# Performance work log

Hardware: AMD Instinct MI355X
Metric: run time of the kernel (lower is better)

Reference implementation:

```python
import jax, jax.numpy as jnp
import numpy as np

DIM = 256
HEADS = 8
WS = 16      # window size
WN = 16      # num windows (img 64x64)
KS = 3
B = 16
IMG = 64


def setup_inputs() -> dict:
    key = jax.random.key(0)
    ks = jax.random.split(key, 12)
    d = DIM
    hid = d // 16  # SE hidden (d >= 64)
    inp = {
        "x": jax.random.normal(ks[0], (B, d, IMG, IMG), dtype=jnp.float32),
        "conv_w": jax.random.normal(ks[1], (WN, d, d, KS, KS), dtype=jnp.float32) * 0.02,
        "wqkv": jax.random.normal(ks[2], (d, 3 * d), dtype=jnp.float32) * 0.02,
        "bqkv": jax.random.normal(ks[3], (3 * d,), dtype=jnp.float32) * 0.02,
        "wout": jax.random.normal(ks[4], (d, d), dtype=jnp.float32) * 0.02,
        "bout": jax.random.normal(ks[5], (d,), dtype=jnp.float32) * 0.02,
        "se_w1": jax.random.normal(ks[6], (WN, hid, d), dtype=jnp.float32) * 0.05,
        "se_b1": jax.random.normal(ks[7], (WN, hid), dtype=jnp.float32) * 0.02,
        "se_w2": jax.random.normal(ks[8], (WN, d, hid), dtype=jnp.float32) * 0.05,
        "se_b2": jax.random.normal(ks[9], (WN, d), dtype=jnp.float32) * 0.02,
        "ln_g": jnp.ones((d,), dtype=jnp.float32),
        "ln_b": jnp.zeros((d,), dtype=jnp.float32),
    }
    return inp


def reference(x, conv_w, wqkv, bqkv, wout, bout, se_w1, se_b1, se_w2, se_b2, ln_g, ln_b):
    Bn, C, H, W = x.shape
    hd = C // HEADS
    scale = hd ** (-0.5)

    # window partition: (WN, B, C, WS, WS), windows in (h_idx, w_idx) row-major order
    xw = x.reshape(Bn, C, H // WS, WS, W // WS, WS).transpose(2, 4, 0, 1, 3, 5)
    xw = xw.reshape(WN, Bn, C, WS, WS)

    # kernel tokens: per-layer weight.view(B, C, -1).permute(0,2,1), cat on axis 1
    last = C * KS * KS // Bn
    kt = conv_w.reshape(WN, Bn, C, last).transpose(1, 0, 3, 2).reshape(Bn, WN * last, C)

    # self-attention over kernel tokens (batch axis becomes dim C after reshape)
    qkv = kt @ wqkv + bqkv                                    # (B, WN*last, 3C)
    qkv = qkv.reshape(C, WN * KS * KS, 3, HEADS, hd).transpose(2, 0, 3, 1, 4)
    q, k, v = qkv[0] * scale, qkv[1], qkv[2]                  # (C, H, T, hd), T = WN*KS*KS
    attn = jax.nn.softmax(jnp.einsum('dhqe,dhke->dhqk', q, k), axis=-1)
    o = jnp.einsum('dhqk,dhke->dhqe', attn, v)
    o = o.transpose(0, 2, 1, 3).reshape(C, WN * KS * KS, C)
    o = o @ wout + bout
    kern = o.reshape(C, WN, KS, KS, C).transpose(1, 0, 4, 2, 3)  # (WN, Cout, Cin, KS, KS)

    # SE gating per window: kernels[i] treated as (batch=C, channels=C, KS, KS)
    pooled = kern.mean(axis=(3, 4))                            # (WN, C, C)
    h = jax.nn.relu(jnp.einsum('wbc,whc->wbh', pooled, se_w1) + se_b1[:, None, :])
    s = jax.nn.sigmoid(jnp.einsum('wbh,wch->wbc', h, se_w2) + se_b2[:, None, :])
    kern = kern * s[:, :, :, None, None]

    # per-window conv as a single grouped conv (groups = WN)
    xg = xw.transpose(1, 0, 2, 3, 4).reshape(Bn, WN * C, WS, WS)
    wg = kern.reshape(WN * C, C, KS, KS)
    yg = jax.lax.conv_general_dilated(xg, wg, (1, 1), ((1, 1), (1, 1)),
                                      feature_group_count=WN)
    yw = yg.reshape(Bn, WN, C, WS, WS).transpose(1, 0, 2, 3, 4)  # (WN, B, C, WS, WS)

    # window reverse
    y = yw.reshape(H // WS, W // WS, Bn, C, WS, WS).transpose(2, 3, 0, 4, 1, 5)
    y = y.reshape(Bn, C, H, W)

    # channel layernorm (eps=1e-5) + residual
    yn = y.transpose(0, 2, 3, 1)
    mu = yn.mean(-1, keepdims=True)
    var = ((yn - mu) ** 2).mean(-1, keepdims=True)
    yn = (yn - mu) / jnp.sqrt(var + 1e-5) * ln_g + ln_b
    return x + yn.transpose(0, 3, 1, 2)
```

## Files before the change

### kernel.cpp

```cpp
#include <hip/hip_runtime.h>

typedef __bf16 bf16;
typedef __bf16 bf16x8 __attribute__((ext_vector_type(8)));
typedef _Float16 f16;
typedef _Float16 f16x8 __attribute__((ext_vector_type(8)));
typedef float f32x4 __attribute__((ext_vector_type(4)));

#define SCALE_Q 0.17677669529663687f
#define KSCALE 64.0f
#define KSCALE_INV 0.015625f

__global__ __launch_bounds__(256) void k_prep_w(const float* __restrict__ wqkv,
                                                const float* __restrict__ wout,
                                                bf16* __restrict__ wqkv_t,
                                                f16* __restrict__ wout_h,
                                                f16* __restrict__ wout_l) {
    int n = blockIdx.x, k = threadIdx.x;
    if (n < 768) {
        wqkv_t[n * 256 + k] = (bf16)wqkv[k * 768 + n];
    } else {
        float f = wout[k * 256 + (n - 768)] * KSCALE;
        f16 hi = (f16)f;
        wout_h[(n - 768) * 256 + k] = hi;
        wout_l[(n - 768) * 256 + k] = (f16)(f - (float)hi);
    }
}

__global__ __launch_bounds__(256) void k_build_kt(const float* __restrict__ conv_w,
                                                  bf16* __restrict__ kt) {
    __shared__ float lds[2304];
    int w = blockIdx.x >> 8, co = blockIdx.x & 255;
    const float* src = conv_w + (size_t)(w * 256 + co) * 2304;
    for (int i = threadIdx.x; i < 2304; i += 256) lds[i] = src[i];
    __syncthreads();
    int b = co >> 4, c0 = (co & 15) << 4;
    size_t rbase = (size_t)(b * 16 + w) * 144;
    for (int i = threadIdx.x; i < 2304; i += 256) {
        int t = i >> 4, m = i & 15;
        kt[(rbase + t) * 256 + c0 + m] = (bf16)lds[m * 144 + t];
    }
}

typedef const __attribute__((address_space(1))) unsigned int* gas_t;
typedef __attribute__((address_space(3))) unsigned int* las_t;

__device__ __forceinline__ void async_copy16(const void* g, void* l) {
    __builtin_amdgcn_global_load_lds((gas_t)g, (las_t)l, 16, 0, 0);
}

__device__ __forceinline__ void mfma_tile_bf16(const bf16* As, const bf16* Bs,
                                               f32x4 acc[4][4]) {
    int lane = threadIdx.x & 63;
    int wave = threadIdx.x >> 6;
    int wm = (wave >> 1) * 64, wn = (wave & 1) * 64;
    int lrow = lane & 15, quad = lane >> 4;
    bf16x8 af[4], bfr[4];
#pragma unroll
    for (int i = 0; i < 4; i++) {
        int r = wm + i * 16 + lrow;
        af[i] = *(const bf16x8*)(As + r * 32 + ((quad ^ ((r >> 1) & 3)) << 3));
        int n = wn + i * 16 + lrow;
        bfr[i] = *(const bf16x8*)(Bs + n * 32 + ((quad ^ ((n >> 1) & 3)) << 3));
    }
#pragma unroll
    for (int i = 0; i < 4; i++)
#pragma unroll
        for (int j = 0; j < 4; j++)
            acc[i][j] = __builtin_amdgcn_mfma_f32_16x16x32_bf16(af[i], bfr[j], acc[i][j], 0, 0, 0);
}

__device__ __forceinline__ void mfma_tile_f16_dual(const f16* As, const f16* Bhs,
                                                   const f16* Bls, f32x4 acc[4][4]) {
    int lane = threadIdx.x & 63;
    int wave = threadIdx.x >> 6;
    int wm = (wave >> 1) * 64, wn = (wave & 1) * 64;
    int lrow = lane & 15, quad = lane >> 4;
    f16x8 af[4], bh[4], bl[4];
#pragma unroll
    for (int i = 0; i < 4; i++) {
        int r = wm + i * 16 + lrow;
        af[i] = *(const f16x8*)(As + r * 32 + ((quad ^ ((r >> 1) & 3)) << 3));
        int n = wn + i * 16 + lrow;
        bh[i] = *(const f16x8*)(Bhs + n * 32 + ((quad ^ ((n >> 1) & 3)) << 3));
        bl[i] = *(const f16x8*)(Bls + n * 32 + ((quad ^ ((n >> 1) & 3)) << 3));
    }
#pragma unroll
    for (int i = 0; i < 4; i++)
#pragma unroll
        for (int j = 0; j < 4; j++) {
            acc[i][j] = __builtin_amdgcn_mfma_f32_16x16x32_f16(af[i], bh[j], acc[i][j], 0, 0, 0);
            acc[i][j] = __builtin_amdgcn_mfma_f32_16x16x32_f16(af[i], bl[j], acc[i][j], 0, 0, 0);
        }
}

__device__ __forceinline__ void mfma_tile_f16_dual8(const f16* As, const f16* Bhs,
                                                    const f16* Bls, f32x4 acc[8][4]) {
    int lane = threadIdx.x & 63;
    int wave = threadIdx.x >> 6;
    int wm = (wave >> 1) * 128, wn = (wave & 1) * 64;
    int lrow = lane & 15, quad = lane >> 4;
    f16x8 af[8], bh[4], bl[4];
#pragma unroll
    for (int i = 0; i < 8; i++) {
        int r = wm + i * 16 + lrow;
        af[i] = *(const f16x8*)(As + r * 32 + ((quad ^ ((r >> 1) & 3)) << 3));
    }
#pragma unroll
    for (int j = 0; j < 4; j++) {
        int n = wn + j * 16 + lrow;
        bh[j] = *(const f16x8*)(Bhs + n * 32 + ((quad ^ ((n >> 1) & 3)) << 3));
        bl[j] = *(const f16x8*)(Bls + n * 32 + ((quad ^ ((n >> 1) & 3)) << 3));
    }
#pragma unroll
    for (int i = 0; i < 8; i++)
#pragma unroll
        for (int j = 0; j < 4; j++) {
            acc[i][j] = __builtin_amdgcn_mfma_f32_16x16x32_f16(af[i], bh[j], acc[i][j], 0, 0, 0);
            acc[i][j] = __builtin_amdgcn_mfma_f32_16x16x32_f16(af[i], bl[j], acc[i][j], 0, 0, 0);
        }
}

__global__ __launch_bounds__(256) void k_gemm_qkv(const bf16* __restrict__ A,
                                                  const bf16* __restrict__ Bt,
                                                  const float* __restrict__ bias,
                                                  bf16* __restrict__ outb,
                                                  int N, int K) {
    __shared__ __align__(16) bf16 As[2][128 * 32];
    __shared__ __align__(16) bf16 Bs[2][128 * 32];
    int m0 = blockIdx.y * 128, n0 = blockIdx.x * 128;
    int t = threadIdx.x, wave = t >> 6, lane = t & 63;
    int chunk0 = wave * 2, chunk1 = chunk0 + 1;
    int row0 = chunk0 * 16 + (lane >> 2), row1 = row0 + 16;
    int sw = ((lane & 3) ^ ((row0 >> 1) & 3)) << 3;
    const unsigned short* Ag = (const unsigned short*)A;
    const unsigned short* Bg = (const unsigned short*)Bt;
    size_t a0 = (size_t)(m0 + row0) * K + sw, a1 = (size_t)(m0 + row1) * K + sw;
    size_t b0 = (size_t)(n0 + row0) * K + sw, b1 = (size_t)(n0 + row1) * K + sw;
    f32x4 acc[4][4] = {};
#define STG_QKV(cur, k0)                                        \
    async_copy16(Ag + a0 + (k0), &As[cur][chunk0 * 512]);       \
    async_copy16(Ag + a1 + (k0), &As[cur][chunk1 * 512]);       \
    async_copy16(Bg + b0 + (k0), &Bs[cur][chunk0 * 512]);       \
    async_copy16(Bg + b1 + (k0), &Bs[cur][chunk1 * 512]);
    STG_QKV(0, 0);
    int cur = 0, NT = K >> 5;
#pragma unroll 1
    for (int it = 0; it < NT; it++) {
        if (it < NT - 1) {
            STG_QKV(cur ^ 1, (it + 1) << 5);
            asm volatile("s_waitcnt vmcnt(4)" ::: "memory");
        } else {
            asm volatile("s_waitcnt vmcnt(0)" ::: "memory");
        }
        __builtin_amdgcn_s_barrier();
        mfma_tile_bf16(As[cur], Bs[cur], acc);
        asm volatile("s_waitcnt lgkmcnt(0)" ::: "memory");
        __builtin_amdgcn_s_barrier();
        cur ^= 1;
    }
#undef STG_QKV
    int wm = (wave >> 1) * 64, wn = (wave & 1) * 64;
    int lrow = lane & 15, quad = lane >> 4;
#pragma unroll
    for (int i = 0; i < 4; i++)
#pragma unroll
        for (int j = 0; j < 4; j++) {
            int col = n0 + wn + j * 16 + lrow;
            float bv = bias[col];
#pragma unroll
            for (int rr = 0; rr < 4; rr++) {
                int row = m0 + wm + i * 16 + quad * 4 + rr;
                float v = acc[i][j][rr] + bv;
                if (col < 256) v *= SCALE_Q;
                outb[(size_t)row * N + col] = (bf16)v;
            }
        }
}

__global__ __launch_bounds__(256) void k_gemm_split2(const f16* __restrict__ Ag_,
                                                     const f16* __restrict__ Bhg,
                                                     const f16* __restrict__ Blg,
                                                     const float* __restrict__ bias,
                                                     float* __restrict__ outf,
                                                     int N, int K) {
    __shared__ __align__(16) f16 As[2][128 * 32];
    __shared__ __align__(16) f16 Bh[2][128 * 32];
    __shared__ __align__(16) f16 Bl[2][128 * 32];
    int m0 = blockIdx.y * 128, n0 = blockIdx.x * 128;
    int t = threadIdx.x, wave = t >> 6, lane = t & 63;
    int chunk0 = wave * 2, chunk1 = chunk0 + 1;
    int row0 = chunk0 * 16 + (lane >> 2), row1 = row0 + 16;
    int sw = ((lane & 3) ^ ((row0 >> 1) & 3)) << 3;
    const unsigned short* Au = (const unsigned short*)Ag_;
    const unsigned short* Bhu = (const unsigned short*)Bhg;
    const unsigned short* Blu = (const unsigned short*)Blg;
    size_t a0 = (size_t)(m0 + row0) * K + sw, a1 = (size_t)(m0 + row1) * K + sw;
    size_t b0 = (size_t)(n0 + row0) * K + sw, b1 = (size_t)(n0 + row1) * K + sw;
    f32x4 acc[4][4] = {};
#define STG_SP2(cur, k0)                                        \
    async_copy16(Au + a0 + (k0), &As[cur][chunk0 * 512]);       \
    async_copy16(Au + a1 + (k0), &As[cur][chunk1 * 512]);       \
    async_copy16(Bhu + b0 + (k0), &Bh[cur][chunk0 * 512]);      \
    async_copy16(Bhu + b1 + (k0), &Bh[cur][chunk1 * 512]);      \
    async_copy16(Blu + b0 + (k0), &Bl[cur][chunk0 * 512]);      \
    async_copy16(Blu + b1 + (k0), &Bl[cur][chunk1 * 512]);
    STG_SP2(0, 0);
    int cur = 0, NT = K >> 5;
#pragma unroll 1
    for (int it = 0; it < NT; it++) {
        if (it < NT - 1) {
            STG_SP2(cur ^ 1, (it + 1) << 5);
            asm volatile("s_waitcnt vmcnt(6)" ::: "memory");
        } else {
            asm volatile("s_waitcnt vmcnt(0)" ::: "memory");
        }
        __builtin_amdgcn_s_barrier();
        mfma_tile_f16_dual(As[cur], Bh[cur], Bl[cur], acc);
        asm volatile("s_waitcnt lgkmcnt(0)" ::: "memory");
        __builtin_amdgcn_s_barrier();
        cur ^= 1;
    }
#undef STG_SP2
    int wm = (wave >> 1) * 64, wn = (wave & 1) * 64;
    int lrow = lane & 15, quad = lane >> 4;
#pragma unroll
    for (int i = 0; i < 4; i++)
#pragma unroll
        for (int j = 0; j < 4; j++) {
            int col = n0 + wn + j * 16 + lrow;
            float bv = bias[col];
#pragma unroll
            for (int rr = 0; rr < 4; rr++) {
                int row = m0 + wm + i * 16 + quad * 4 + rr;
                outf[(size_t)row * N + col] = acc[i][j][rr] * KSCALE_INV + bv;
            }
        }
}

__global__ __launch_bounds__(256) void k_attn(const bf16* __restrict__ qkv,
                                              f16* __restrict__ o16) {
    __shared__ bf16 Qs[144 * 32];
    __shared__ bf16 Ks[144 * 32];
    __shared__ f16 Vt[32 * 160];
    __shared__ f16 Ps[4 * 16 * 168];
    int d = blockIdx.x >> 3, h = blockIdx.x & 7;
    const bf16* base = qkv + (size_t)d * 144 * 768 + h * 32;
    int t = threadIdx.x;

    for (int i = t; i < 512; i += 256) Vt[(i >> 4) * 160 + 144 + (i & 15)] = (f16)0.f;
    for (int i = t; i < 576; i += 256) {
        int row = i >> 2, part = i & 3;
        const bf16* rp = base + (size_t)row * 768;
        uint4 vq = *(const uint4*)(rp + (part << 3));
        uint4 vk = *(const uint4*)(rp + 256 + (part << 3));
        int sw = ((part ^ (row & 3)) << 3);
        *(uint4*)(Qs + row * 32 + sw) = vq;
        *(uint4*)(Ks + row * 32 + sw) = vk;
        bf16x8 v8 = *(const bf16x8*)(rp + 512 + (part << 3));
#pragma unroll
        for (int j = 0; j < 8; j++) Vt[(part * 8 + j) * 160 + row] = (f16)(float)v8[j];
    }
    __syncthreads();

    int wave = t >> 6, lane = t & 63;
    int lrow = lane & 15, quad = lane >> 4;
    f16* Pw = Ps + wave * 16 * 168;
    for (int i = lane; i < 256; i += 64) Pw[(i >> 4) * 168 + 144 + (i & 15)] = (f16)0.f;

    bf16x8 kf[9];
#pragma unroll
    for (int nt = 0; nt < 9; nt++) {
        int r = nt * 16 + lrow;
        kf[nt] = *(const bf16x8*)(Ks + r * 32 + ((quad ^ (r & 3)) << 3));
    }

    for (int mt = wave; mt < 9; mt += 4) {
        int qr = mt * 16 + lrow;
        bf16x8 qf = *(const bf16x8*)(Qs + qr * 32 + ((quad ^ (qr & 3)) << 3));
        f32x4 s[9];
#pragma unroll
        for (int nt = 0; nt < 9; nt++) {
            f32x4 z = {0.f, 0.f, 0.f, 0.f};
            s[nt] = __builtin_amdgcn_mfma_f32_16x16x32_bf16(qf, kf[nt], z, 0, 0, 0);
        }
        f32x4 mx = s[0];
#pragma unroll
        for (int nt = 1; nt < 9; nt++)
#pragma unroll
            for (int c = 0; c < 4; c++) mx[c] = fmaxf(mx[c], s[nt][c]);
#pragma unroll
        for (int off = 1; off < 16; off <<= 1)
#pragma unroll
            for (int c = 0; c < 4; c++) mx[c] = fmaxf(mx[c], __shfl_xor(mx[c], off));
        f32x4 sm = {0.f, 0.f, 0.f, 0.f};
#pragma unroll
        for (int nt = 0; nt < 9; nt++)
#pragma unroll
            for (int c = 0; c < 4; c++) {
                float e = __expf(s[nt][c] - mx[c]);
                s[nt][c] = e;
                sm[c] += e;
            }
#pragma unroll
        for (int off = 1; off < 16; off <<= 1)
#pragma unroll
            for (int c = 0; c < 4; c++) sm[c] += __shfl_xor(sm[c], off);
        f32x4 inv;
#pragma unroll
        for (int c = 0; c < 4; c++) inv[c] = 1.f / sm[c];
#pragma unroll
        for (int nt = 0; nt < 9; nt++)
#pragma unroll
            for (int c = 0; c < 4; c++)
                Pw[(quad * 4 + c) * 168 + nt * 16 + lrow] = (f16)(s[nt][c] * inv[c]);

        f32x4 o0 = {0.f, 0.f, 0.f, 0.f}, o1 = {0.f, 0.f, 0.f, 0.f};
#pragma unroll
        for (int kt = 0; kt < 5; kt++) {
            f16x8 pf = *(const f16x8*)(Pw + lrow * 168 + kt * 32 + quad * 8);
            f16x8 v0 = *(const f16x8*)(Vt + lrow * 160 + kt * 32 + quad * 8);
            f16x8 v1 = *(const f16x8*)(Vt + (16 + lrow) * 160 + kt * 32 + quad * 8);
            o0 = __builtin_amdgcn_mfma_f32_16x16x32_f16(pf, v0, o0, 0, 0, 0);
            o1 = __builtin_amdgcn_mfma_f32_16x16x32_f16(pf, v1, o1, 0, 0, 0);
        }
        size_t ro = ((size_t)d * 144 + mt * 16) * 256 + h * 32;
#pragma unroll
        for (int c = 0; c < 4; c++) {
            size_t rr = ro + (size_t)(quad * 4 + c) * 256;
            o16[rr + lrow] = (f16)o0[c];
            o16[rr + 16 + lrow] = (f16)o1[c];
        }
    }
}

__global__ __launch_bounds__(256) void k_se_scale(const float* __restrict__ kern,
                                                  const float* __restrict__ w1,
                                                  const float* __restrict__ b1,
                                                  const float* __restrict__ w2,
                                                  const float* __restrict__ b2,
                                                  f16* __restrict__ kern_hi,
                                                  f16* __restrict__ kern_lo) {
    __shared__ float pooled[256];
    __shared__ float hbuf[16];
    int w = blockIdx.x >> 8, Co = blockIdx.x & 255;
    int ci = threadIdx.x;
    const float* kb = kern + (size_t)(Co * 16 + w) * 9 * 256;
    float v9[9];
    float pv = 0.f;
#pragma unroll
    for (int k9 = 0; k9 < 9; k9++) { v9[k9] = kb[k9 * 256 + ci]; pv += v9[k9]; }
    pooled[ci] = pv * (1.f / 9.f);
    __syncthreads();
    {
        int hid = ci >> 4, l16 = ci & 15;
        const float* w1p = w1 + (size_t)(w * 16 + hid) * 256;
        float hs = 0.f;
#pragma unroll
        for (int c = l16; c < 256; c += 16) hs += pooled[c] * w1p[c];
        hs += __shfl_xor(hs, 1);
        hs += __shfl_xor(hs, 2);
        hs += __shfl_xor(hs, 4);
        hs += __shfl_xor(hs, 8);
        if (l16 == 0) hbuf[hid] = fmaxf(hs + b1[w * 16 + hid], 0.f);
    }
    __syncthreads();
    const float* w2p = w2 + (size_t)(w * 256 + ci) * 16;
    float ss = b2[w * 256 + ci];
#pragma unroll
    for (int j = 0; j < 16; j++) ss += hbuf[j] * w2p[j];
    float s = (1.f / (1.f + __expf(-ss))) * KSCALE;
    size_t outo = (size_t)(w * 256 + Co) * 2304;
    f16* khi = kern_hi + outo;
    f16* klo = kern_lo + outo;
#pragma unroll
    for (int k9 = 0; k9 < 9; k9++) {
        float f = v9[k9] * s;
        f16 hi = (f16)f;
        khi[k9 * 256 + ci] = hi;
        klo[k9 * 256 + ci] = (f16)(f - (float)hi);
    }
}

__global__ __launch_bounds__(256) void k_zero(uint4* __restrict__ p, int n4) {
    int stride = gridDim.x * 256;
    for (int i = blockIdx.x * 256 + threadIdx.x; i < n4; i += stride)
        p[i] = uint4{0u, 0u, 0u, 0u};
}

__global__ __launch_bounds__(256) void k_fill_xcl(const float* __restrict__ x,
                                                  f16* __restrict__ xcl) {
    int bx = blockIdx.x;
    int b = bx >> 6, gy = bx & 63;
    int wrow = gy >> 4, py = gy & 15;
    int ci = threadIdx.x;
    const float* xp = x + ((size_t)(b * 256 + ci) * 64 + gy) * 64;
    for (int wx = 0; wx < 4; wx++) {
        int w = wrow * 4 + wx;
        size_t o = (((size_t)(w * 16 + b) * 18 + py + 1) * 18 + 1) * 256 + ci;
#pragma unroll
        for (int px = 0; px < 16; px++)
            xcl[o + (size_t)px * 256] = (f16)xp[wx * 16 + px];
    }
}

__global__ __launch_bounds__(256, 2) void k_conv_gemm(const f16* __restrict__ xcl,
                                                      const f16* __restrict__ kern_hi,
                                                      const f16* __restrict__ kern_lo,
                                                      float* __restrict__ y) {
    __shared__ __align__(16) f16 As[2][256 * 32];
    __shared__ __align__(16) f16 Bh[2][128 * 32];
    __shared__ __align__(16) f16 Bl[2][128 * 32];
    int f = blockIdx.x;
    int xcd = f & 7, i5 = f >> 3;
    int w = xcd * 2 + (i5 >> 5);
    int rem = i5 & 31;
    int by = rem >> 1;
    int n0 = (rem & 1) * 128;
    int m0 = by * 256;
    const unsigned short* xw = (const unsigned short*)(xcl + (size_t)w * 16 * 18 * 18 * 256);
    const unsigned short* Bthu = (const unsigned short*)(kern_hi + (size_t)w * 256 * 2304);
    const unsigned short* Btlu = (const unsigned short*)(kern_lo + (size_t)w * 256 * 2304);
    int t = threadIdx.x, wave = t >> 6, lane = t & 63;
    int sw = ((lane & 3) ^ ((lane >> 3) & 3)) << 3;
    size_t aA[4];
#pragma unroll
    for (int c = 0; c < 4; c++) {
        int row = (wave * 4 + c) * 16 + (lane >> 2);
        int py = row >> 4, px = row & 15;
        aA[c] = ((size_t)(by * 18 + py) * 18 + px) * 256 + sw;
    }
    int rb0 = (wave * 2) * 16 + (lane >> 2), rb1 = rb0 + 16;
    size_t bB0 = (size_t)(n0 + rb0) * 2304 + sw;
    size_t bB1 = (size_t)(n0 + rb1) * 2304 + sw;
    f32x4 acc[8][4] = {};
#define STG_CONV(cur, k0)                                                      \
    {                                                                          \
        int k9_ = (k0) >> 8;                                                   \
        int koff_ = ((k9_ / 3) * 18 + (k9_ % 3)) * 256 + ((k0) & 255);         \
        async_copy16(xw + aA[0] + koff_, &As[cur][(wave * 4 + 0) * 512]);      \
        async_copy16(xw + aA[1] + koff_, &As[cur][(wave * 4 + 1) * 512]);      \
        async_copy16(xw + aA[2] + koff_, &As[cur][(wave * 4 + 2) * 512]);      \
        async_copy16(xw + aA[3] + koff_, &As[cur][(wave * 4 + 3) * 512]);      \
        async_copy16(Bthu + bB0 + (k0), &Bh[cur][(wave * 2 + 0) * 512]);       \
        async_copy16(Bthu + bB1 + (k0), &Bh[cur][(wave * 2 + 1) * 512]);       \
        async_copy16(Btlu + bB0 + (k0), &Bl[cur][(wave * 2 + 0) * 512]);       \
        async_copy16(Btlu + bB1 + (k0), &Bl[cur][(wave * 2 + 1) * 512]);       \
    }
    STG_CONV(0, 0);
    int cur = 0;
#pragma unroll 1
    for (int it = 0; it < 72; it++) {
        if (it < 71) {
            STG_CONV(cur ^ 1, (it + 1) << 5);
            asm volatile("s_waitcnt vmcnt(8)" ::: "memory");
        } else {
            asm volatile("s_waitcnt vmcnt(0)" ::: "memory");
        }
        __builtin_amdgcn_s_barrier();
        mfma_tile_f16_dual8(As[cur], Bh[cur], Bl[cur], acc);
        asm volatile("s_waitcnt lgkmcnt(0)" ::: "memory");
        __builtin_amdgcn_s_barrier();
        cur ^= 1;
    }
#undef STG_CONV
    int lrow = lane & 15, quad = lane >> 4;
    int wm = (wave >> 1) * 128, wn = (wave & 1) * 64;
    float* yw = y + (size_t)w * 4096 * 256;
#pragma unroll
    for (int i = 0; i < 8; i++)
#pragma unroll
        for (int j = 0; j < 4; j++) {
            int col = n0 + wn + j * 16 + lrow;
#pragma unroll
            for (int rr = 0; rr < 4; rr++) {
                int row = m0 + wm + i * 16 + quad * 4 + rr;
                yw[(size_t)row * 256 + col] = acc[i][j][rr] * KSCALE_INV;
            }
        }
}

__global__ __launch_bounds__(256) void k_ln_res(const float* __restrict__ y,
                                                const float* __restrict__ x,
                                                const float* __restrict__ g,
                                                const float* __restrict__ be,
                                                float* __restrict__ out) {
    int bx = blockIdx.x;
    int b = bx >> 6, gy = bx & 63;
    int t = threadIdx.x;
    int j = t >> 2, sub = t & 3;
    int w = (gy >> 4) * 4 + (j >> 4);
    int p = (gy & 15) * 16 + (j & 15);
    const float* yp = y + ((size_t)w * 4096 + b * 256 + p) * 256 + sub * 64;
    float vals[64];
    float sum = 0.f, sq = 0.f;
#pragma unroll
    for (int c = 0; c < 64; c++) {
        float v = yp[c];
        vals[c] = v;
        sum += v; sq += v * v;
    }
    sum += __shfl_xor(sum, 1); sq += __shfl_xor(sq, 1);
    sum += __shfl_xor(sum, 2); sq += __shfl_xor(sq, 2);
    float mean = sum * (1.f / 256.f);
    float var = sq * (1.f / 256.f) - mean * mean;
    float rstd = rsqrtf(var + 1e-5f);
    const float* xp = x + ((size_t)(b * 256 + sub * 64) * 64 + gy) * 64 + j;
    float* op = out + ((size_t)(b * 256 + sub * 64) * 64 + gy) * 64 + j;
#pragma unroll
    for (int c = 0; c < 64; c++) {
        int cc = sub * 64 + c;
        op[(size_t)c * 4096] = (vals[c] - mean) * rstd * g[cc] + be[cc] + xp[(size_t)c * 4096];
    }
}

extern "C" void kernel_launch(void* const* d_in, const int* in_sizes, int n_in,
                              void* d_out, int out_size, void* d_ws, size_t ws_size,
                              hipStream_t stream) {
    const float* x      = (const float*)d_in[0];
    const float* conv_w = (const float*)d_in[1];
    const float* wqkv   = (const float*)d_in[2];
    const float* bqkv   = (const float*)d_in[3];
    const float* wout   = (const float*)d_in[4];
    const float* bout   = (const float*)d_in[5];
    const float* se_w1  = (const float*)d_in[6];
    const float* se_b1  = (const float*)d_in[7];
    const float* se_w2  = (const float*)d_in[8];
    const float* se_b2  = (const float*)d_in[9];
    const float* ln_g   = (const float*)d_in[10];
    const float* ln_b   = (const float*)d_in[11];
    float* out = (float*)d_out;

    char* ws = (char*)d_ws;
    bf16*  kt      = (bf16*)(ws + 0);
    f16*   o16     = (f16*)(ws + 0);
    f16*   kern_hi = (f16*)(ws + 0);
    f16*   kern_lo = (f16*)(ws + 18874368);
    bf16*  wqkv_t  = (bf16*)(ws + 37748736);
    f16*   wout_h  = (f16*)(ws + 38141952);
    f16*   wout_l  = (f16*)(ws + 38273024);
    f16*   xcl     = (f16*)(ws + 38404096);
    bf16*  qkv     = (bf16*)(ws + 80871424);
    float* kern_f  = (float*)(ws + 80871424);
    float* y       = (float*)(ws + 80871424);

    k_prep_w<<<1024, 256, 0, stream>>>(wqkv, wout, wqkv_t, wout_h, wout_l);
    k_build_kt<<<4096, 256, 0, stream>>>(conv_w, kt);
    k_gemm_qkv<<<dim3(6, 288), 256, 0, stream>>>(kt, wqkv_t, bqkv, qkv, 768, 256);
    k_attn<<<2048, 256, 0, stream>>>(qkv, o16);
    k_gemm_split2<<<dim3(2, 288), 256, 0, stream>>>(o16, wout_h, wout_l, bout, kern_f, 256, 256);
    k_se_scale<<<4096, 256, 0, stream>>>(kern_f, se_w1, se_b1, se_w2, se_b2, kern_hi, kern_lo);
    k_zero<<<2048, 256, 0, stream>>>((uint4*)xcl, 42467328 / 16);
    k_fill_xcl<<<1024, 256, 0, stream>>>(x, xcl);
    k_conv_gemm<<<512, 256, 0, stream>>>(xcl, kern_hi, kern_lo, y);
    k_ln_res<<<1024, 256, 0, stream>>>(y, x, ln_g, ln_b, out);
}
```

Before: 480.4 us.

## Zero only halo of padded input, pad LDS transpose, restage layernorm via LDS

```diff
diff --git a/kernel.cpp b/kernel.cpp
--- a/kernel.cpp
+++ b/kernel.cpp
@@ -28,16 +28,19 @@
 
 __global__ __launch_bounds__(256) void k_build_kt(const float* __restrict__ conv_w,
                                                   bf16* __restrict__ kt) {
-    __shared__ float lds[2304];
+    __shared__ float lds[16 * 145];
     int w = blockIdx.x >> 8, co = blockIdx.x & 255;
     const float* src = conv_w + (size_t)(w * 256 + co) * 2304;
-    for (int i = threadIdx.x; i < 2304; i += 256) lds[i] = src[i];
+    for (int i = threadIdx.x; i < 2304; i += 256) {
+        int m = i / 144, tt = i - m * 144;
+        lds[m * 145 + tt] = src[i];
+    }
     __syncthreads();
     int b = co >> 4, c0 = (co & 15) << 4;
     size_t rbase = (size_t)(b * 16 + w) * 144;
     for (int i = threadIdx.x; i < 2304; i += 256) {
         int t = i >> 4, m = i & 15;
-        kt[(rbase + t) * 256 + c0 + m] = (bf16)lds[m * 144 + t];
+        kt[(rbase + t) * 256 + c0 + m] = (bf16)lds[m * 145 + t];
     }
 }
 
@@ -381,10 +384,18 @@
     }
 }
 
-__global__ __launch_bounds__(256) void k_zero(uint4* __restrict__ p, int n4) {
-    int stride = gridDim.x * 256;
-    for (int i = blockIdx.x * 256 + threadIdx.x; i < n4; i += stride)
-        p[i] = uint4{0u, 0u, 0u, 0u};
+__global__ __launch_bounds__(256) void k_zero_pad(f16* __restrict__ xcl) {
+    int wb = blockIdx.x;
+    f16* base = xcl + (size_t)wb * 18 * 18 * 256;
+    int ci = threadIdx.x;
+#pragma unroll 1
+    for (int i = 0; i < 68; i++) {
+        int py, px;
+        if (i < 18) { py = 0; px = i; }
+        else if (i < 36) { py = 17; px = i - 18; }
+        else { int k = i - 36; py = 1 + (k >> 1); px = (k & 1) * 17; }
+        base[((size_t)py * 18 + px) * 256 + ci] = (f16)0.f;
+    }
 }
 
 __global__ __launch_bounds__(256) void k_fill_xcl(const float* __restrict__ x,
@@ -484,32 +495,44 @@
                                                 const float* __restrict__ g,
                                                 const float* __restrict__ be,
                                                 float* __restrict__ out) {
+    __shared__ float vbuf[32 * 257];
+    __shared__ float stats[32][2];
     int bx = blockIdx.x;
-    int b = bx >> 6, gy = bx & 63;
+    int half = bx & 1, gy = (bx >> 1) & 63, b = bx >> 7;
     int t = threadIdx.x;
-    int j = t >> 2, sub = t & 3;
-    int w = (gy >> 4) * 4 + (j >> 4);
-    int p = (gy & 15) * 16 + (j & 15);
-    const float* yp = y + ((size_t)w * 4096 + b * 256 + p) * 256 + sub * 64;
-    float vals[64];
+    int j = t >> 3, sub = t & 7;
+    int gx = half * 32 + j;
+    int w = (gy >> 4) * 4 + (gx >> 4);
+    int p = (gy & 15) * 16 + (gx & 15);
+    const float* yp = y + ((size_t)w * 4096 + b * 256 + p) * 256 + sub * 32;
     float sum = 0.f, sq = 0.f;
 #pragma unroll
-    for (int c = 0; c < 64; c++) {
+    for (int c = 0; c < 32; c++) {
         float v = yp[c];
-        vals[c] = v;
+        vbuf[j * 257 + sub * 32 + c] = v;
         sum += v; sq += v * v;
     }
     sum += __shfl_xor(sum, 1); sq += __shfl_xor(sq, 1);
     sum += __shfl_xor(sum, 2); sq += __shfl_xor(sq, 2);
-    float mean = sum * (1.f / 256.f);
-    float var = sq * (1.f / 256.f) - mean * mean;
-    float rstd = rsqrtf(var + 1e-5f);
-    const float* xp = x + ((size_t)(b * 256 + sub * 64) * 64 + gy) * 64 + j;
-    float* op = out + ((size_t)(b * 256 + sub * 64) * 64 + gy) * 64 + j;
-#pragma unroll
-    for (int c = 0; c < 64; c++) {
-        int cc = sub * 64 + c;
-        op[(size_t)c * 4096] = (vals[c] - mean) * rstd * g[cc] + be[cc] + xp[(size_t)c * 4096];
+    sum += __shfl_xor(sum, 4); sq += __shfl_xor(sq, 4);
+    if (sub == 0) {
+        float mean = sum * (1.f / 256.f);
+        float var = sq * (1.f / 256.f) - mean * mean;
+        stats[j][0] = mean;
+        stats[j][1] = rsqrtf(var + 1e-5f);
+    }
+    __syncthreads();
+    int wv = t >> 6, lane = t & 63;
+    int chp = lane >> 5, lgx = lane & 31;
+    float mu = stats[lgx][0], rstd = stats[lgx][1];
+    const float* xrow = x + ((size_t)(b * 256) * 64 + gy) * 64 + half * 32 + lgx;
+    float* orow = out + ((size_t)(b * 256) * 64 + gy) * 64 + half * 32 + lgx;
+#pragma unroll 4
+    for (int it = 0; it < 32; it++) {
+        int ch = wv * 64 + it * 2 + chp;
+        float v = vbuf[lgx * 257 + ch];
+        float r = (v - mu) * rstd * g[ch] + be[ch] + xrow[(size_t)ch * 4096];
+        orow[(size_t)ch * 4096] = r;
     }
 }
 
@@ -549,8 +572,8 @@
     k_attn<<<2048, 256, 0, stream>>>(qkv, o16);
     k_gemm_split2<<<dim3(2, 288), 256, 0, stream>>>(o16, wout_h, wout_l, bout, kern_f, 256, 256);
     k_se_scale<<<4096, 256, 0, stream>>>(kern_f, se_w1, se_b1, se_w2, se_b2, kern_hi, kern_lo);
-    k_zero<<<2048, 256, 0, stream>>>((uint4*)xcl, 42467328 / 16);
+    k_zero_pad<<<256, 256, 0, stream>>>(xcl);
     k_fill_xcl<<<1024, 256, 0, stream>>>(x, xcl);
     k_conv_gemm<<<512, 256, 0, stream>>>(xcl, kern_hi, kern_lo, y);
-    k_ln_res<<<1024, 256, 0, stream>>>(y, x, ln_g, ln_b, out);
-}
+    k_ln_res<<<2048, 256, 0, stream>>>(y, x, ln_g, ln_b, out);
+}
```

New measurement: 474.1 us. About the same (-1.3%).
